# Kernel tuning notes

Hardware: AMD Instinct MI355X
Metric: run time of the kernel (lower is better)

Reference implementation:

```python
import jax, jax.numpy as jnp
import numpy as np

ALG = 8  # octonion algebra dimension
_TRIPLES = [(1,2,3),(1,4,5),(1,7,6),(2,4,6),(2,5,7),(3,4,7),(3,6,5)]

def _oct_table():
    # Cayley multiplication table: e_i * e_j = S[i,j] * e_{K[i,j]}
    K = np.zeros((8,8), np.int64); S = np.zeros((8,8), np.int64)
    K[0,:] = np.arange(8); S[0,:] = 1
    K[:,0] = np.arange(8); S[:,0] = 1
    for i in range(1,8):
        K[i,i] = 0; S[i,i] = -1
    for (a,b,c) in _TRIPLES:
        for x,y,z in ((a,b,c),(b,c,a),(c,a,b)):
            K[x,y] = z; S[x,y] = 1
            K[y,x] = z; S[y,x] = -1
    return K, S

_K, _S = _oct_table()

def _ternary(w):
    # BitNet-style absmean ternary quantization (STE is irrelevant for fwd)
    scale = jnp.mean(jnp.abs(w)) + 1e-8
    wq = jnp.clip(jnp.round(w / scale), -1.0, 1.0) * scale
    return w + jax.lax.stop_gradient(wq - w)

def _oct_big(w):
    # w: [8, din8, dout8] -> structured dense [8*din8, 8*dout8]
    # out_k = sum_{i,j: e_i e_j = s e_k} s * x_i @ W_j  (64 static blocks)
    din8, dout8 = w.shape[1], w.shape[2]
    big = jnp.zeros((8, din8, 8, dout8), w.dtype)
    for i in range(8):
        for j in range(8):
            big = big.at[i, :, int(_K[i, j]), :].set(float(_S[i, j]) * w[j])
    return big.reshape(8 * din8, 8 * dout8)

def _oct_linear(x, w):
    return x @ _oct_big(_ternary(w))

def setup_inputs() -> dict:
    key = jax.random.key(0)
    k1, k2, k3, k4 = jax.random.split(key, 4)
    B, T, D = 8, 4096, 768
    H = 2048  # int(2*4*768/3) rounded up to multiple of 8
    d8, h8 = D // ALG, H // ALG
    x = jax.random.normal(k1, (B, T, D), dtype=jnp.float32)
    w_gate = 0.02 * jax.random.normal(k2, (ALG, d8, h8), dtype=jnp.float32)
    w_up   = 0.02 * jax.random.normal(k3, (ALG, d8, h8), dtype=jnp.float32)
    w_down = 0.02 * jax.random.normal(k4, (ALG, h8, d8), dtype=jnp.float32)
    return {"x": x, "w_gate": w_gate, "w_up": w_up, "w_down": w_down}

def reference(x, w_gate, w_up, w_down):
    gate = _oct_linear(x, w_gate)          # [B,T,H]
    up   = _oct_linear(x, w_up)            # [B,T,H]
    h    = jax.nn.silu(gate) * up          # SwiGLU gate
    return _oct_linear(h, w_down)          # [B,T,D]
```

## Files before the change

### kernel.cpp

```cpp
#include <hip/hip_runtime.h>
#include <hip/hip_bf16.h>

typedef unsigned short u16;
typedef unsigned int u32;
typedef float f32x4 __attribute__((ext_vector_type(4)));
typedef __bf16 bf16x8 __attribute__((ext_vector_type(8)));

#define AS1 __attribute__((address_space(1)))
#define AS3 __attribute__((address_space(3)))

#define MTOT 32768
#define DK   768
#define HN   2048

__constant__ signed char J_TAB[64] = {
  0,1,2,3,4,5,6,7,
  1,0,3,2,5,4,7,6,
  2,3,0,1,6,7,4,5,
  3,2,1,0,7,6,5,4,
  4,5,6,7,0,1,2,3,
  5,4,7,6,1,0,3,2,
  6,7,4,5,2,3,0,1,
  7,6,5,4,3,2,1,0};
__constant__ signed char S_TAB[64] = {
   1, 1, 1, 1, 1, 1, 1, 1,
  -1, 1,-1, 1,-1, 1, 1,-1,
  -1, 1, 1,-1,-1,-1, 1, 1,
  -1,-1, 1, 1,-1, 1,-1, 1,
  -1, 1, 1, 1, 1,-1,-1,-1,
  -1,-1, 1,-1, 1, 1, 1,-1,
  -1,-1,-1, 1, 1,-1, 1, 1,
  -1, 1,-1,-1, 1, 1,-1, 1};

__device__ __forceinline__ u16 f2bf(float f) {
  u32 x = __float_as_uint(f);
  x += 0x7fffu + ((x >> 16) & 1u);
  return (u16)(x >> 16);
}

__device__ __forceinline__ void gload_lds16(const void* g, void* l) {
  __builtin_amdgcn_global_load_lds((AS1 void*)(g), (AS3 void*)(l), 16, 0, 0);
}

template <int ROWS>
__device__ __forceinline__ void stage_tile(const u16* __restrict__ src, int ldk,
                                           u16* lds, int tid) {
#pragma unroll
  for (int f0 = 0; f0 < ROWS * 8; f0 += 256) {
    int flat = f0 + tid;
    int row = flat >> 3;
    int c = (flat & 7) ^ (row & 7);
    gload_lds16(src + row * ldk + c * 8, lds + (f0 + (tid & 192)) * 8);
  }
}

__device__ __forceinline__ bf16x8 frag64(const u16* lds, int row, int cbase) {
  int c = cbase ^ (row & 7);
  return *(const bf16x8*)(lds + row * 64 + c * 8);
}

__global__ void scales1_kernel(const float* __restrict__ w0,
                               const float* __restrict__ w1,
                               const float* __restrict__ w2,
                               float* __restrict__ partials) {
  __shared__ float red[256];
  const int t = blockIdx.x / 192;
  const int chunk = blockIdx.x % 192;
  const float* w = (t == 0) ? w0 : (t == 1) ? w1 : w2;
  const float4* w4 = (const float4*)(w + chunk * 1024);
  float4 v = w4[threadIdx.x];
  red[threadIdx.x] = fabsf(v.x) + fabsf(v.y) + fabsf(v.z) + fabsf(v.w);
  __syncthreads();
  for (int off = 128; off; off >>= 1) {
    if (threadIdx.x < off) red[threadIdx.x] += red[threadIdx.x + off];
    __syncthreads();
  }
  if (threadIdx.x == 0) partials[blockIdx.x] = red[0];
}

__global__ void scales2_kernel(const float* __restrict__ partials,
                               float* __restrict__ scales) {
  __shared__ float red[256];
  float s = (threadIdx.x < 192) ? partials[blockIdx.x * 192 + threadIdx.x] : 0.f;
  red[threadIdx.x] = s;
  __syncthreads();
  for (int off = 128; off; off >>= 1) {
    if (threadIdx.x < off) red[threadIdx.x] += red[threadIdx.x + off];
    __syncthreads();
  }
  if (threadIdx.x == 0) scales[blockIdx.x] = red[0] / 196608.f + 1e-8f;
}

__global__ void build_big_kernel(const float* __restrict__ w,
                                 const float* __restrict__ scales, int sidx,
                                 int A, int B, u16* __restrict__ dst) {
  int idx = blockIdx.x * 256 + threadIdx.x;
  int K8 = 8 * A;
  int n = idx / K8;
  int k = idx - n * K8;
  int i = k / A, a = k - i * A;
  int c = n / B, b = n - c * B;
  float scale = scales[sidx];
  int j = J_TAB[i * 8 + c];
  float q = rintf(w[(j * A + a) * B + b] / scale);
  q = fminf(1.f, fmaxf(-1.f, q));
  dst[idx] = f2bf(q * (float)S_TAB[i * 8 + c]);
}

__global__ void cvt_x_kernel(const float* __restrict__ x, u16* __restrict__ xb) {
  int gid = blockIdx.x * 256 + threadIdx.x;
  const float4* x4 = (const float4*)x;
  float4 v0 = x4[gid * 2], v1 = x4[gid * 2 + 1];
  uint4 o;
  o.x = (u32)f2bf(v0.x) | ((u32)f2bf(v0.y) << 16);
  o.y = (u32)f2bf(v0.z) | ((u32)f2bf(v0.w) << 16);
  o.z = (u32)f2bf(v1.x) | ((u32)f2bf(v1.y) << 16);
  o.w = (u32)f2bf(v1.z) | ((u32)f2bf(v1.w) << 16);
  ((uint4*)xb)[gid] = o;
}

__global__ __launch_bounds__(256) void gemm1_kernel(
    const u16* __restrict__ xb, const u16* __restrict__ wg,
    const u16* __restrict__ wu, const float* __restrict__ scales,
    u16* __restrict__ h) {
  __shared__ __align__(16) u16 lA[128 * 64];
  __shared__ __align__(16) u16 lG[64 * 64];
  __shared__ __align__(16) u16 lU[64 * 64];
  const int tid = threadIdx.x;
  const int bn = blockIdx.x & 31;
  const int bm = blockIdx.x >> 5;
  const int m0 = bm * 128, n0 = bn * 64;
  const int lane = tid & 63, wave = tid >> 6;
  const int wm = wave >> 1, wn = wave & 1;
  const int l15 = lane & 15, quad = lane >> 4;

  f32x4 accG[4][2] = {};
  f32x4 accU[4][2] = {};

  const u16* aSrc = xb + m0 * DK;
  const u16* gSrc = wg + n0 * DK;
  const u16* uSrc = wu + n0 * DK;

  for (int k0 = 0; k0 < DK; k0 += 64) {
    stage_tile<128>(aSrc + k0, DK, lA, tid);
    stage_tile<64>(gSrc + k0, DK, lG, tid);
    stage_tile<64>(uSrc + k0, DK, lU, tid);
    __syncthreads();
#pragma unroll
    for (int ks = 0; ks < 2; ++ks) {
      const int cb = ks * 4 + quad;
      bf16x8 af[4], gf[2], uf[2];
#pragma unroll
      for (int mi = 0; mi < 4; ++mi)
        af[mi] = frag64(lA, wm * 64 + mi * 16 + l15, cb);
#pragma unroll
      for (int ni = 0; ni < 2; ++ni) {
        gf[ni] = frag64(lG, wn * 32 + ni * 16 + l15, cb);
        uf[ni] = frag64(lU, wn * 32 + ni * 16 + l15, cb);
      }
#pragma unroll
      for (int mi = 0; mi < 4; ++mi)
#pragma unroll
        for (int ni = 0; ni < 2; ++ni) {
          accG[mi][ni] = __builtin_amdgcn_mfma_f32_16x16x32_bf16(
              af[mi], gf[ni], accG[mi][ni], 0, 0, 0);
          accU[mi][ni] = __builtin_amdgcn_mfma_f32_16x16x32_bf16(
              af[mi], uf[ni], accU[mi][ni], 0, 0, 0);
        }
    }
    __syncthreads();
  }

  const float sg = scales[0], su = scales[1];
#pragma unroll
  for (int mi = 0; mi < 4; ++mi)
#pragma unroll
    for (int ni = 0; ni < 2; ++ni)
#pragma unroll
      for (int r = 0; r < 4; ++r) {
        int m = m0 + wm * 64 + mi * 16 + quad * 4 + r;
        int n = n0 + wn * 32 + ni * 16 + l15;
        float g = accG[mi][ni][r] * sg;
        float u = accU[mi][ni][r] * su;
        float hv = g / (1.f + __expf(-g)) * u;
        h[m * HN + n] = f2bf(hv);
      }
}

__global__ __launch_bounds__(256) void gemm2_kernel(
    const u16* __restrict__ h, const u16* __restrict__ wd,
    const float* __restrict__ scales, float* __restrict__ out) {
  __shared__ __align__(16) u16 lA[128 * 64];
  __shared__ __align__(16) u16 lB[128 * 64];
  const int tid = threadIdx.x;
  const int bn = blockIdx.x % 6;
  const int bm = blockIdx.x / 6;
  const int m0 = bm * 128, n0 = bn * 128;
  const int lane = tid & 63, wave = tid >> 6;
  const int wm = wave >> 1, wn = wave & 1;
  const int l15 = lane & 15, quad = lane >> 4;

  f32x4 acc[4][4] = {};

  const u16* aSrc = h + m0 * HN;
  const u16* bSrc = wd + n0 * HN;

  for (int k0 = 0; k0 < HN; k0 += 64) {
    stage_tile<128>(aSrc + k0, HN, lA, tid);
    stage_tile<128>(bSrc + k0, HN, lB, tid);
    __syncthreads();
#pragma unroll
    for (int ks = 0; ks < 2; ++ks) {
      const int cb = ks * 4 + quad;
      bf16x8 af[4], bf[4];
#pragma unroll
      for (int mi = 0; mi < 4; ++mi)
        af[mi] = frag64(lA, wm * 64 + mi * 16 + l15, cb);
#pragma unroll
      for (int ni = 0; ni < 4; ++ni)
        bf[ni] = frag64(lB, wn * 64 + ni * 16 + l15, cb);
#pragma unroll
      for (int mi = 0; mi < 4; ++mi)
#pragma unroll
        for (int ni = 0; ni < 4; ++ni)
          acc[mi][ni] = __builtin_amdgcn_mfma_f32_16x16x32_bf16(
              af[mi], bf[ni], acc[mi][ni], 0, 0, 0);
    }
    __syncthreads();
  }

  const float sd = scales[2];
#pragma unroll
  for (int mi = 0; mi < 4; ++mi)
#pragma unroll
    for (int ni = 0; ni < 4; ++ni)
#pragma unroll
      for (int r = 0; r < 4; ++r) {
        int m = m0 + wm * 64 + mi * 16 + quad * 4 + r;
        int n = n0 + wn * 64 + ni * 16 + l15;
        out[m * DK + n] = acc[mi][ni][r] * sd;
      }
}

extern "C" void kernel_launch(void* const* d_in, const int* in_sizes, int n_in,
                              void* d_out, int out_size, void* d_ws, size_t ws_size,
                              hipStream_t stream) {
  const float* x      = (const float*)d_in[0];
  const float* w_gate = (const float*)d_in[1];
  const float* w_up   = (const float*)d_in[2];
  const float* w_down = (const float*)d_in[3];
  float* out = (float*)d_out;

  char* ws = (char*)d_ws;
  float* scales   = (float*)ws;
  float* partials = (float*)(ws + 256);
  u16* wg = (u16*)(ws + 4096);
  u16* wu = (u16*)(ws + 4096 + 1u * 3145728u);
  u16* wd = (u16*)(ws + 4096 + 2u * 3145728u);
  u16* xb = (u16*)(ws + 4096 + 3u * 3145728u);
  u16* h  = (u16*)(ws + 4096 + 3u * 3145728u + 50331648u);

  scales1_kernel<<<576, 256, 0, stream>>>(w_gate, w_up, w_down, partials);
  scales2_kernel<<<3, 256, 0, stream>>>(partials, scales);
  build_big_kernel<<<6144, 256, 0, stream>>>(w_gate, scales, 0, 96, 256, wg);
  build_big_kernel<<<6144, 256, 0, stream>>>(w_up,   scales, 1, 96, 256, wu);
  build_big_kernel<<<6144, 256, 0, stream>>>(w_down, scales, 2, 256, 96, wd);
  cvt_x_kernel<<<12288, 256, 0, stream>>>(x, xb);
  gemm1_kernel<<<8192, 256, 0, stream>>>(xb, wg, wu, scales, h);
  gemm2_kernel<<<1536, 256, 0, stream>>>(h, wd, scales, out);
}
```

Before: 597.4 us.

## Rewrite GEMMs as 256x256 double-buffered pipelined tiles with interleaved gate/up weights

Both GEMMs move to 256x256 output tiles with 8 waves and double-buffered LDS. Global-to-LDS loads for the next k-tile are interleaved with MFMA phases using explicit vmcnt waits, barriers and setprio. The gate and up weights are stored interleaved in 16-row groups so gemm1 runs as a single GEMM over a fused matrix, and block indices are remapped for cache locality. The aim is to hide memory latency and raise operand reuse per LDS load. The cost is 128 KB of LDS per block and a large register footprint, which limits occupancy.

```diff
diff --git a/kernel.cpp b/kernel.cpp
--- a/kernel.cpp
+++ b/kernel.cpp
@@ -42,21 +42,152 @@
   __builtin_amdgcn_global_load_lds((AS1 void*)(g), (AS3 void*)(l), 16, 0, 0);
 }
 
-template <int ROWS>
-__device__ __forceinline__ void stage_tile(const u16* __restrict__ src, int ldk,
+#define VMW(N) do { __builtin_amdgcn_sched_barrier(0); \
+  asm volatile("s_waitcnt vmcnt(" #N ")" ::: "memory"); \
+  __builtin_amdgcn_sched_barrier(0); } while (0)
+#define BAR() do { __builtin_amdgcn_sched_barrier(0); \
+  __builtin_amdgcn_s_barrier(); \
+  __builtin_amdgcn_sched_barrier(0); } while (0)
+
+template <int LDK>
+__device__ __forceinline__ void stage_half(const u16* __restrict__ src,
                                            u16* lds, int tid) {
 #pragma unroll
-  for (int f0 = 0; f0 < ROWS * 8; f0 += 256) {
+  for (int f0 = 0; f0 < 1024; f0 += 512) {
     int flat = f0 + tid;
     int row = flat >> 3;
     int c = (flat & 7) ^ (row & 7);
-    gload_lds16(src + row * ldk + c * 8, lds + (f0 + (tid & 192)) * 8);
-  }
-}
-
-__device__ __forceinline__ bf16x8 frag64(const u16* lds, int row, int cbase) {
-  int c = cbase ^ (row & 7);
-  return *(const bf16x8*)(lds + row * 64 + c * 8);
+    gload_lds16(src + row * LDK + c * 8, lds + (f0 + (tid & ~63)) * 8);
+  }
+}
+
+template <int LDK, bool SA, bool SB, int VM>
+__device__ __forceinline__ void ktile4(
+    const u16* lAp, const u16* lBp, u16* lAn, u16* lBn,
+    const u16* __restrict__ aStage, const u16* __restrict__ bStage,
+    int tid, int arow, int brow, int c0, int c1, f32x4 (&acc)[8][4]) {
+  bf16x8 afr[4][2], bfr[4][2];
+#pragma unroll
+  for (int mi = 0; mi < 4; ++mi) {
+    const u16* p = lAp + (arow + mi * 16) * 64;
+    afr[mi][0] = *(const bf16x8*)(p + c0);
+    afr[mi][1] = *(const bf16x8*)(p + c1);
+  }
+#pragma unroll
+  for (int ni = 0; ni < 2; ++ni) {
+    const u16* p = lBp + (brow + ni * 16) * 64;
+    bfr[ni][0] = *(const bf16x8*)(p + c0);
+    bfr[ni][1] = *(const bf16x8*)(p + c1);
+  }
+  if constexpr (SA) stage_half<LDK>(aStage, lAn, tid);
+  BAR();
+  __builtin_amdgcn_s_setprio(1);
+#pragma unroll
+  for (int mi = 0; mi < 4; ++mi)
+#pragma unroll
+    for (int ni = 0; ni < 2; ++ni) {
+      acc[mi][ni] = __builtin_amdgcn_mfma_f32_16x16x32_bf16(
+          afr[mi][0], bfr[ni][0], acc[mi][ni], 0, 0, 0);
+      acc[mi][ni] = __builtin_amdgcn_mfma_f32_16x16x32_bf16(
+          afr[mi][1], bfr[ni][1], acc[mi][ni], 0, 0, 0);
+    }
+  __builtin_amdgcn_s_setprio(0);
+  BAR();
+#pragma unroll
+  for (int ni = 2; ni < 4; ++ni) {
+    const u16* p = lBp + (brow + ni * 16) * 64;
+    bfr[ni][0] = *(const bf16x8*)(p + c0);
+    bfr[ni][1] = *(const bf16x8*)(p + c1);
+  }
+  if constexpr (SA) stage_half<LDK>(aStage + 128 * LDK, lAn + 128 * 64, tid);
+  BAR();
+  __builtin_amdgcn_s_setprio(1);
+#pragma unroll
+  for (int mi = 0; mi < 4; ++mi)
+#pragma unroll
+    for (int ni = 2; ni < 4; ++ni) {
+      acc[mi][ni] = __builtin_amdgcn_mfma_f32_16x16x32_bf16(
+          afr[mi][0], bfr[ni][0], acc[mi][ni], 0, 0, 0);
+      acc[mi][ni] = __builtin_amdgcn_mfma_f32_16x16x32_bf16(
+          afr[mi][1], bfr[ni][1], acc[mi][ni], 0, 0, 0);
+    }
+  __builtin_amdgcn_s_setprio(0);
+  BAR();
+#pragma unroll
+  for (int mi = 0; mi < 4; ++mi) {
+    const u16* p = lAp + (arow + 64 + mi * 16) * 64;
+    afr[mi][0] = *(const bf16x8*)(p + c0);
+    afr[mi][1] = *(const bf16x8*)(p + c1);
+  }
+  if constexpr (SB) stage_half<LDK>(bStage, lBn, tid);
+  BAR();
+  __builtin_amdgcn_s_setprio(1);
+#pragma unroll
+  for (int mi = 0; mi < 4; ++mi)
+#pragma unroll
+    for (int ni = 2; ni < 4; ++ni) {
+      acc[4 + mi][ni] = __builtin_amdgcn_mfma_f32_16x16x32_bf16(
+          afr[mi][0], bfr[ni][0], acc[4 + mi][ni], 0, 0, 0);
+      acc[4 + mi][ni] = __builtin_amdgcn_mfma_f32_16x16x32_bf16(
+          afr[mi][1], bfr[ni][1], acc[4 + mi][ni], 0, 0, 0);
+    }
+  __builtin_amdgcn_s_setprio(0);
+  BAR();
+  if constexpr (SB) stage_half<LDK>(bStage + 128 * LDK, lBn + 128 * 64, tid);
+  if constexpr (VM == 4) VMW(4);
+  else if constexpr (VM == 0) VMW(0);
+  BAR();
+  __builtin_amdgcn_s_setprio(1);
+#pragma unroll
+  for (int mi = 0; mi < 4; ++mi)
+#pragma unroll
+    for (int ni = 0; ni < 2; ++ni) {
+      acc[4 + mi][ni] = __builtin_amdgcn_mfma_f32_16x16x32_bf16(
+          afr[mi][0], bfr[ni][0], acc[4 + mi][ni], 0, 0, 0);
+      acc[4 + mi][ni] = __builtin_amdgcn_mfma_f32_16x16x32_bf16(
+          afr[mi][1], bfr[ni][1], acc[4 + mi][ni], 0, 0, 0);
+    }
+  __builtin_amdgcn_s_setprio(0);
+  BAR();
+}
+
+template <int NK, int LDK>
+__device__ __forceinline__ void gemm_core(const u16* __restrict__ aSrc,
+                                          const u16* __restrict__ bSrc, int tid,
+                                          u16* lA0, u16* lA1, u16* lB0, u16* lB1,
+                                          f32x4 (&acc)[8][4]) {
+  const int lane = tid & 63;
+  const int wave = tid >> 6;
+  const int wm = wave >> 2, wn = wave & 3;
+  const int l15 = lane & 15, quad = (lane >> 4) & 3;
+  const int arow = wm * 128 + l15;
+  const int brow = wn * 64 + l15;
+  const int c0 = (quad ^ (l15 & 7)) * 8;
+  const int c1 = ((quad + 4) ^ (l15 & 7)) * 8;
+
+  stage_half<LDK>(aSrc, lA0, tid);
+  stage_half<LDK>(aSrc + 128 * LDK, lA0 + 128 * 64, tid);
+  stage_half<LDK>(bSrc, lB0, tid);
+  stage_half<LDK>(bSrc + 128 * LDK, lB0 + 128 * 64, tid);
+  stage_half<LDK>(bSrc + 64, lB1, tid);
+  stage_half<LDK>(bSrc + 64 + 128 * LDK, lB1 + 128 * 64, tid);
+  VMW(4);
+  BAR();
+
+#pragma unroll 1
+  for (int i = 0; i < NK / 2 - 1; ++i) {
+    ktile4<LDK, true, true, 4>(lA0, lB0, lA1, lB0,
+                               aSrc + (2 * i + 1) * 64, bSrc + (2 * i + 2) * 64,
+                               tid, arow, brow, c0, c1, acc);
+    ktile4<LDK, true, true, 4>(lA1, lB1, lA0, lB1,
+                               aSrc + (2 * i + 2) * 64, bSrc + (2 * i + 3) * 64,
+                               tid, arow, brow, c0, c1, acc);
+  }
+  ktile4<LDK, true, false, 0>(lA0, lB0, lA1, lB0,
+                              aSrc + (NK - 1) * 64, nullptr,
+                              tid, arow, brow, c0, c1, acc);
+  ktile4<LDK, false, false, -1>(lA1, lB1, lA0, lB1, nullptr, nullptr,
+                                tid, arow, brow, c0, c1, acc);
 }
 
 __global__ void scales1_kernel(const float* __restrict__ w0,
@@ -93,7 +224,7 @@
 
 __global__ void build_big_kernel(const float* __restrict__ w,
                                  const float* __restrict__ scales, int sidx,
-                                 int A, int B, u16* __restrict__ dst) {
+                                 int A, int B, int ilv, u16* __restrict__ dst) {
   int idx = blockIdx.x * 256 + threadIdx.x;
   int K8 = 8 * A;
   int n = idx / K8;
@@ -104,7 +235,8 @@
   int j = J_TAB[i * 8 + c];
   float q = rintf(w[(j * A + a) * B + b] / scale);
   q = fminf(1.f, fmaxf(-1.f, q));
-  dst[idx] = f2bf(q * (float)S_TAB[i * 8 + c]);
+  int nd = (ilv < 0) ? n : (((n & ~15) << 1) | (ilv << 4) | (n & 15));
+  dst[nd * K8 + k] = f2bf(q * (float)S_TAB[i * 8 + c]);
 }
 
 __global__ void cvt_x_kernel(const float* __restrict__ x, u16* __restrict__ xb) {
@@ -119,127 +251,72 @@
   ((uint4*)xb)[gid] = o;
 }
 
-__global__ __launch_bounds__(256) void gemm1_kernel(
-    const u16* __restrict__ xb, const u16* __restrict__ wg,
-    const u16* __restrict__ wu, const float* __restrict__ scales,
-    u16* __restrict__ h) {
-  __shared__ __align__(16) u16 lA[128 * 64];
-  __shared__ __align__(16) u16 lG[64 * 64];
-  __shared__ __align__(16) u16 lU[64 * 64];
+__global__ __launch_bounds__(512, 2) void gemm1_kernel(
+    const u16* __restrict__ xb, const u16* __restrict__ wgu,
+    const float* __restrict__ scales, u16* __restrict__ h) {
+  __shared__ __align__(16) u16 lA0[256 * 64], lA1[256 * 64];
+  __shared__ __align__(16) u16 lB0[256 * 64], lB1[256 * 64];
   const int tid = threadIdx.x;
-  const int bn = blockIdx.x & 31;
-  const int bm = blockIdx.x >> 5;
-  const int m0 = bm * 128, n0 = bn * 64;
+  const int logical = (blockIdx.x & 7) * 256 + (blockIdx.x >> 3);
+  const int bn = logical & 15;
+  const int bm = logical >> 4;
+  const int m0 = bm * 256, n0 = bn * 256;
+
+  f32x4 acc[8][4] = {};
+  gemm_core<12, DK>(xb + (size_t)m0 * DK, wgu + (size_t)n0 * DK, tid,
+                    lA0, lA1, lB0, lB1, acc);
+
   const int lane = tid & 63, wave = tid >> 6;
-  const int wm = wave >> 1, wn = wave & 1;
+  const int wm = wave >> 2, wn = wave & 3;
   const int l15 = lane & 15, quad = lane >> 4;
-
-  f32x4 accG[4][2] = {};
-  f32x4 accU[4][2] = {};
-
-  const u16* aSrc = xb + m0 * DK;
-  const u16* gSrc = wg + n0 * DK;
-  const u16* uSrc = wu + n0 * DK;
-
-  for (int k0 = 0; k0 < DK; k0 += 64) {
-    stage_tile<128>(aSrc + k0, DK, lA, tid);
-    stage_tile<64>(gSrc + k0, DK, lG, tid);
-    stage_tile<64>(uSrc + k0, DK, lU, tid);
-    __syncthreads();
-#pragma unroll
-    for (int ks = 0; ks < 2; ++ks) {
-      const int cb = ks * 4 + quad;
-      bf16x8 af[4], gf[2], uf[2];
-#pragma unroll
-      for (int mi = 0; mi < 4; ++mi)
-        af[mi] = frag64(lA, wm * 64 + mi * 16 + l15, cb);
-#pragma unroll
-      for (int ni = 0; ni < 2; ++ni) {
-        gf[ni] = frag64(lG, wn * 32 + ni * 16 + l15, cb);
-        uf[ni] = frag64(lU, wn * 32 + ni * 16 + l15, cb);
+  const float sg = scales[0], su = scales[1];
+  const int hb = bn * 8 + wn * 2;
+#pragma unroll
+  for (int mi = 0; mi < 8; ++mi)
+#pragma unroll
+    for (int pr = 0; pr < 2; ++pr) {
+      const int hc = (hb + pr) * 16 + l15;
+#pragma unroll
+      for (int r = 0; r < 4; ++r) {
+        int m = m0 + wm * 128 + mi * 16 + quad * 4 + r;
+        float g = acc[mi][2 * pr][r] * sg;
+        float u = acc[mi][2 * pr + 1][r] * su;
+        float hv = g / (1.f + __expf(-g)) * u;
+        h[(size_t)m * HN + hc] = f2bf(hv);
       }
-#pragma unroll
-      for (int mi = 0; mi < 4; ++mi)
-#pragma unroll
-        for (int ni = 0; ni < 2; ++ni) {
-          accG[mi][ni] = __builtin_amdgcn_mfma_f32_16x16x32_bf16(
-              af[mi], gf[ni], accG[mi][ni], 0, 0, 0);
-          accU[mi][ni] = __builtin_amdgcn_mfma_f32_16x16x32_bf16(
-              af[mi], uf[ni], accU[mi][ni], 0, 0, 0);
-        }
-    }
-    __syncthreads();
-  }
-
-  const float sg = scales[0], su = scales[1];
-#pragma unroll
-  for (int mi = 0; mi < 4; ++mi)
-#pragma unroll
-    for (int ni = 0; ni < 2; ++ni)
-#pragma unroll
-      for (int r = 0; r < 4; ++r) {
-        int m = m0 + wm * 64 + mi * 16 + quad * 4 + r;
-        int n = n0 + wn * 32 + ni * 16 + l15;
-        float g = accG[mi][ni][r] * sg;
-        float u = accU[mi][ni][r] * su;
-        float hv = g / (1.f + __expf(-g)) * u;
-        h[m * HN + n] = f2bf(hv);
-      }
-}
-
-__global__ __launch_bounds__(256) void gemm2_kernel(
+    }
+}
+
+__global__ __launch_bounds__(512, 2) void gemm2_kernel(
     const u16* __restrict__ h, const u16* __restrict__ wd,
     const float* __restrict__ scales, float* __restrict__ out) {
-  __shared__ __align__(16) u16 lA[128 * 64];
-  __shared__ __align__(16) u16 lB[128 * 64];
+  __shared__ __align__(16) u16 lA0[256 * 64], lA1[256 * 64];
+  __shared__ __align__(16) u16 lB0[256 * 64], lB1[256 * 64];
   const int tid = threadIdx.x;
-  const int bn = blockIdx.x % 6;
-  const int bm = blockIdx.x / 6;
-  const int m0 = bm * 128, n0 = bn * 128;
+  const int logical = (blockIdx.x & 7) * 48 + (blockIdx.x >> 3);
+  const int bn = logical % 3;
+  const int bm = logical / 3;
+  const int m0 = bm * 256, n0 = bn * 256;
+
+  f32x4 acc[8][4] = {};
+  gemm_core<32, HN>(h + (size_t)m0 * HN, wd + (size_t)n0 * HN, tid,
+                    lA0, lA1, lB0, lB1, acc);
+
   const int lane = tid & 63, wave = tid >> 6;
-  const int wm = wave >> 1, wn = wave & 1;
+  const int wm = wave >> 2, wn = wave & 3;
   const int l15 = lane & 15, quad = lane >> 4;
-
-  f32x4 acc[4][4] = {};
-
-  const u16* aSrc = h + m0 * HN;
-  const u16* bSrc = wd + n0 * HN;
-
-  for (int k0 = 0; k0 < HN; k0 += 64) {
-    stage_tile<128>(aSrc + k0, HN, lA, tid);
-    stage_tile<128>(bSrc + k0, HN, lB, tid);
-    __syncthreads();
-#pragma unroll
-    for (int ks = 0; ks < 2; ++ks) {
-      const int cb = ks * 4 + quad;
-      bf16x8 af[4], bf[4];
-#pragma unroll
-      for (int mi = 0; mi < 4; ++mi)
-        af[mi] = frag64(lA, wm * 64 + mi * 16 + l15, cb);
-#pragma unroll
-      for (int ni = 0; ni < 4; ++ni)
-        bf[ni] = frag64(lB, wn * 64 + ni * 16 + l15, cb);
-#pragma unroll
-      for (int mi = 0; mi < 4; ++mi)
-#pragma unroll
-        for (int ni = 0; ni < 4; ++ni)
-          acc[mi][ni] = __builtin_amdgcn_mfma_f32_16x16x32_bf16(
-              af[mi], bf[ni], acc[mi][ni], 0, 0, 0);
-    }
-    __syncthreads();
-  }
-
   const float sd = scales[2];
 #pragma unroll
-  for (int mi = 0; mi < 4; ++mi)
-#pragma unroll
-    for (int ni = 0; ni < 4; ++ni)
+  for (int mi = 0; mi < 8; ++mi)
+#pragma unroll
+    for (int ni = 0; ni < 4; ++ni) {
+      const int n = n0 + wn * 64 + ni * 16 + l15;
 #pragma unroll
       for (int r = 0; r < 4; ++r) {
-        int m = m0 + wm * 64 + mi * 16 + quad * 4 + r;
-        int n = n0 + wn * 64 + ni * 16 + l15;
-        out[m * DK + n] = acc[mi][ni][r] * sd;
+        int m = m0 + wm * 128 + mi * 16 + quad * 4 + r;
+        out[(size_t)m * DK + n] = acc[mi][ni][r] * sd;
       }
+    }
 }
 
 extern "C" void kernel_launch(void* const* d_in, const int* in_sizes, int n_in,
@@ -254,18 +331,17 @@
   char* ws = (char*)d_ws;
   float* scales   = (float*)ws;
   float* partials = (float*)(ws + 256);
-  u16* wg = (u16*)(ws + 4096);
-  u16* wu = (u16*)(ws + 4096 + 1u * 3145728u);
-  u16* wd = (u16*)(ws + 4096 + 2u * 3145728u);
-  u16* xb = (u16*)(ws + 4096 + 3u * 3145728u);
-  u16* h  = (u16*)(ws + 4096 + 3u * 3145728u + 50331648u);
+  u16* wgu = (u16*)(ws + 4096);
+  u16* wd  = (u16*)(ws + 4096 + 6291456u);
+  u16* xb  = (u16*)(ws + 4096 + 9437184u);
+  u16* h   = (u16*)(ws + 4096 + 9437184u + 50331648u);
 
   scales1_kernel<<<576, 256, 0, stream>>>(w_gate, w_up, w_down, partials);
   scales2_kernel<<<3, 256, 0, stream>>>(partials, scales);
-  build_big_kernel<<<6144, 256, 0, stream>>>(w_gate, scales, 0, 96, 256, wg);
-  build_big_kernel<<<6144, 256, 0, stream>>>(w_up,   scales, 1, 96, 256, wu);
-  build_big_kernel<<<6144, 256, 0, stream>>>(w_down, scales, 2, 256, 96, wd);
+  build_big_kernel<<<6144, 256, 0, stream>>>(w_gate, scales, 0, 96, 256, 0, wgu);
+  build_big_kernel<<<6144, 256, 0, stream>>>(w_up,   scales, 1, 96, 256, 1, wgu);
+  build_big_kernel<<<6144, 256, 0, stream>>>(w_down, scales, 2, 256, 96, -1, wd);
   cvt_x_kernel<<<12288, 256, 0, stream>>>(x, xb);
-  gemm1_kernel<<<8192, 256, 0, stream>>>(xb, wg, wu, scales, h);
-  gemm2_kernel<<<1536, 256, 0, stream>>>(h, wd, scales, out);
-}
+  gemm1_kernel<<<2048, 512, 0, stream>>>(xb, wgu, scales, h);
+  gemm2_kernel<<<384, 512, 0, stream>>>(h, wd, scales, out);
+}
```

Measured after the change: 577.2 us. 3.4% less time.
